# Optimization experiments

Hardware: AMD Instinct MI355X
Metric: run time of the kernel (lower is better)

Reference implementation:

```python
import jax, jax.numpy as jnp
import numpy as np

DIM = 256
NUM_RFS = 256
OUT_DIM = 1024
N = 65536
M = 0.001


def setup_inputs() -> dict:
    key = jax.random.key(0)
    k1, k2, k3, k4, k5, k6 = jax.random.split(key, 6)
    x = jax.random.normal(k1, (N, DIM), dtype=jnp.float32)
    input_weights = jax.random.normal(k2, (OUT_DIM, DIM), dtype=jnp.float32)
    b = jax.random.normal(k3, (OUT_DIM,), dtype=jnp.float32)
    # projection matrix: normal(mean=0, std=0.02, size=(num_rfs, dim))
    proj = 0.02 * jax.random.normal(k4, (NUM_RFS, DIM), dtype=jnp.float32)
    # xis are complex points of the random-feature construction; keep small for exp stability
    xis_real = 0.1 * jax.random.normal(k5, (NUM_RFS,), dtype=jnp.float32)
    xis_imag = 0.1 * jax.random.normal(k6, (NUM_RFS,), dtype=jnp.float32)
    return {"x": x, "input_weights": input_weights, "b": b, "proj": proj,
            "xis_real": xis_real, "xis_imag": xis_imag}


def _asym_feats(xw, xis, proj, bias, is_weight):
    """create_asym_feats with a_fun/b_fun = identity, A_fun/B_fun = exp(xi*b).
    xw: (rows, DIM) float; xis: (NUM_RFS,) complex64; proj: (NUM_RFS, DIM) float.
    Returns (rows, NUM_RFS) complex64."""
    ab = xis  # ab_fun is identity -> ab_coeffs = xis
    scale = np.sqrt(1.0 + 4.0 * M).astype(np.float32)
    # renorm_gs[i] = sqrt(1+4M) * ab[i] * gs[i]  -> (NUM_RFS, DIM) complex
    renorm_gs = scale * ab[:, None] * proj.astype(jnp.complex64)
    # dot_products = xw_c @ renorm_gs.T  -> (rows, NUM_RFS) complex
    dot = jnp.einsum('nd,rd->nr', xw.astype(jnp.complex64), renorm_gs)
    sq = jnp.sum(xw * xw, axis=-1)  # (rows,)
    # correction: outer(sq/2, ab*ab) + M*||g_i||^2 (broadcast over rows)
    corr = (sq[:, None] * 0.5) * (ab * ab)[None, :]
    corr = corr + M * jnp.sum(proj * proj, axis=-1)[None, :]
    feats = jnp.exp(dot - corr) * np.float32(1.0 / np.sqrt(NUM_RFS))
    if is_weight:
        # AB_coeffs[j, i] = exp(xis[i] * bias[j])
        AB = jnp.exp(xis[None, :] * bias[:, None].astype(jnp.complex64))
        feats = AB * feats
    return feats


def reference(x, input_weights, b, proj, xis_real, xis_imag):
    xis = (xis_real + 1j * xis_imag).astype(jnp.complex64)
    # normalize=False path: scale weights and bias by dim**-0.25 at init time
    inv4 = np.float32(1.0 / DIM ** 0.25)
    w = input_weights * inv4
    bb = b * inv4
    c = np.float32((1.0 / np.sqrt(2.0)) * (1.0 + 4.0 * M) ** (DIM / 4.0))
    # precomputed weight features (parameter of the module)
    w_plus = _asym_feats(w, xis, proj, bb, is_weight=True)
    w_minus = _asym_feats(w, -xis, proj, bb, is_weight=True)
    weights = c * jnp.concatenate([w_plus, w_minus], axis=-1)  # (OUT_DIM, 2R) complex
    # forward: x scaled by 1/dim (normalize=False)
    xs = x * np.float32(1.0 / DIM)
    f_plus = _asym_feats(xs, xis, proj, bb, is_weight=False)
    f_minus = _asym_feats(xs, -xis, proj, bb, is_weight=False)
    feat = c * jnp.concatenate([f_plus, f_minus], axis=-1)  # (N, 2R) complex
    # (feat @ weights.T).real
    out = jnp.einsum('nr,or->no', feat, weights).real
    return out
```

## Files before the change

kernel.cpp:

```cpp
#include <hip/hip_runtime.h>
#include <cmath>
#include <cstdint>

#define NROWS 65536
#define DIMN  256
#define NRF   256
#define OUTD  1024
#define KDIM  1024
#define MCOEF 0.001f

typedef __bf16 v8bf __attribute__((ext_vector_type(8)));
typedef float  v4f  __attribute__((ext_vector_type(4)));

__device__ __forceinline__ unsigned short f2bf(float f) {
  unsigned int u = __float_as_uint(f);
  u += 0x7fffu + ((u >> 16) & 1u);
  return (unsigned short)(u >> 16);
}

__device__ __forceinline__ void async_copy16(const void* g, void* l) {
  __builtin_amdgcn_global_load_lds(
      (const __attribute__((address_space(1))) void*)g,
      (__attribute__((address_space(3))) void*)l, 16, 0, 0);
}

__global__ __launch_bounds__(256) void prep_rows(
    const float* __restrict__ src, unsigned short* __restrict__ dst,
    float* __restrict__ sqout, float scl, int rows) {
  int row  = blockIdx.x * 4 + (threadIdx.x >> 6);
  int lane = threadIdx.x & 63;
  if (row >= rows) return;
  float4 v = ((const float4*)(src + (size_t)row * DIMN))[lane];
  v.x *= scl; v.y *= scl; v.z *= scl; v.w *= scl;
  float ss = v.x * v.x + v.y * v.y + v.z * v.z + v.w * v.w;
  ushort4 o;
  o.x = f2bf(v.x); o.y = f2bf(v.y); o.z = f2bf(v.z); o.w = f2bf(v.w);
  ((ushort4*)(dst + (size_t)row * DIMN))[lane] = o;
#pragma unroll
  for (int off = 32; off > 0; off >>= 1) ss += __shfl_down(ss, off, 64);
  if (lane == 0) sqout[row] = ss;
}

__global__ __launch_bounds__(64) void prep_rf(
    const float* __restrict__ proj, unsigned short* __restrict__ projbf,
    float* __restrict__ mg2) {
  int i = blockIdx.x;
  int lane = threadIdx.x;
  float4 v = ((const float4*)(proj + (size_t)i * DIMN))[lane];
  ushort4 o;
  o.x = f2bf(v.x); o.y = f2bf(v.y); o.z = f2bf(v.z); o.w = f2bf(v.w);
  ((ushort4*)(projbf + (size_t)i * DIMN))[lane] = o;
  float ss = v.x * v.x + v.y * v.y + v.z * v.z + v.w * v.w;
#pragma unroll
  for (int off = 32; off > 0; off >>= 1) ss += __shfl_down(ss, off, 64);
  if (lane == 0) mg2[i] = MCOEF * ss;
}

__global__ __launch_bounds__(256) void fused_features(
    const unsigned short* __restrict__ Am,
    const float* __restrict__ sq,
    const float* __restrict__ bias,
    float bscl,
    const float* __restrict__ xr_g, const float* __restrict__ xi_g,
    const float* __restrict__ mg2_g,
    const unsigned short* __restrict__ projbf,
    unsigned short* __restrict__ Fout,
    float sR, float sI, float scaleC) {
  __shared__ __align__(16) unsigned short As[64 * 32];
  __shared__ __align__(16) unsigned short Bs[256 * 32];
  __shared__ float xr_s[256], xi_s[256], c1_s[256], c2_s[256], mg2_s[256];
  __shared__ float sq_s[64], bias_s[64];

  int t = threadIdx.x;
  int lane = t & 63;
  int w = t >> 6;
  int blockRow = blockIdx.x * 64;

  {
    float a = xr_g[t], b = xi_g[t];
    xr_s[t] = a; xi_s[t] = b;
    c1_s[t] = a * a - b * b;
    c2_s[t] = 2.f * a * b;
    mg2_s[t] = mg2_g[t];
  }
  if (t < 64) {
    int r = blockRow + t;
    sq_s[t] = sq[r];
    bias_s[t] = bias ? bias[r] * bscl : 0.f;
  }

  v4f acc[4][4];
#pragma unroll
  for (int a = 0; a < 4; a++)
#pragma unroll
    for (int b = 0; b < 4; b++)
#pragma unroll
      for (int q = 0; q < 4; q++) acc[a][b][q] = 0.f;

  for (int kb = 0; kb < DIMN; kb += 32) {
    {
      int idx = t;
      int row = idx >> 2, kc = (idx & 3) * 8;
      async_copy16(Am + (size_t)(blockRow + row) * DIMN + kb + kc,
                   As + (idx & ~63) * 8);
    }
#pragma unroll
    for (int r = 0; r < 4; r++) {
      int idx = r * 256 + t;
      int row = idx >> 2, kc = (idx & 3) * 8;
      async_copy16(projbf + (size_t)row * DIMN + kb + kc,
                   Bs + (idx & ~63) * 8);
    }
    __syncthreads();
    v8bf af[4], bfv[4];
#pragma unroll
    for (int mi = 0; mi < 4; mi++)
      af[mi] = *(const v8bf*)&As[(mi * 16 + (lane & 15)) * 32 + (lane >> 4) * 8];
#pragma unroll
    for (int ni = 0; ni < 4; ni++)
      bfv[ni] = *(const v8bf*)&Bs[(w * 64 + ni * 16 + (lane & 15)) * 32 + (lane >> 4) * 8];
#pragma unroll
    for (int mi = 0; mi < 4; mi++)
#pragma unroll
      for (int ni = 0; ni < 4; ni++)
        acc[mi][ni] = __builtin_amdgcn_mfma_f32_16x16x32_bf16(
            af[mi], bfv[ni], acc[mi][ni], 0, 0, 0);
    __syncthreads();
  }

#pragma unroll
  for (int mi = 0; mi < 4; mi++) {
#pragma unroll
    for (int ni = 0; ni < 4; ni++) {
#pragma unroll
      for (int reg = 0; reg < 4; reg++) {
        int rloc = mi * 16 + (lane >> 4) * 4 + reg;
        int i    = w * 64 + ni * 16 + (lane & 15);
        float px = acc[mi][ni][reg];
        float tt = scaleC * px + bias_s[rloc];
        float u  = 0.5f * sq_s[rloc];
        float aa = u * c1_s[i] + mg2_s[i];
        float bb = u * c2_s[i];
        float txr = tt * xr_s[i];
        float txi = tt * xi_s[i];
        float erp = __expf(txr - aa);
        float erm = __expf(-txr - aa);
        float s1, cc1, s2, cc2;
        __sincosf(txi - bb, &s1, &cc1);
        __sincosf(txi + bb, &s2, &cc2);
        unsigned short* o = Fout + (size_t)(blockRow + rloc) * KDIM;
        o[i]             = f2bf(sR * erp * cc1);
        o[NRF + i]       = f2bf(sR * erm * cc2);
        o[2 * NRF + i]   = f2bf(sI * erp * s1);
        o[3 * NRF + i]   = f2bf(-sI * erm * s2);
      }
    }
  }
}

__global__ __launch_bounds__(256) void gemm_bt(
    const unsigned short* __restrict__ A,
    const unsigned short* __restrict__ B,
    float* __restrict__ C) {
  __shared__ __align__(16) unsigned short As[128 * 32];
  __shared__ __align__(16) unsigned short Bs[128 * 32];
  int t = threadIdx.x;
  int lane = t & 63;
  int w = t >> 6;
  int wm = w >> 1, wn = w & 1;
  size_t bm = (size_t)blockIdx.y * 128;
  size_t bn = (size_t)blockIdx.x * 128;

  v4f acc[4][4];
#pragma unroll
  for (int a = 0; a < 4; a++)
#pragma unroll
    for (int b = 0; b < 4; b++)
#pragma unroll
      for (int q = 0; q < 4; q++) acc[a][b][q] = 0.f;

  for (int kb = 0; kb < KDIM; kb += 32) {
#pragma unroll
    for (int r = 0; r < 2; r++) {
      int idx = r * 256 + t;
      int row = idx >> 2, kc = (idx & 3) * 8;
      async_copy16(A + (bm + row) * KDIM + kb + kc, As + (idx & ~63) * 8);
      async_copy16(B + (bn + row) * KDIM + kb + kc, Bs + (idx & ~63) * 8);
    }
    __syncthreads();
    v8bf af[4], bfv[4];
#pragma unroll
    for (int mi = 0; mi < 4; mi++)
      af[mi] = *(const v8bf*)&As[(wm * 64 + mi * 16 + (lane & 15)) * 32 + (lane >> 4) * 8];
#pragma unroll
    for (int ni = 0; ni < 4; ni++)
      bfv[ni] = *(const v8bf*)&Bs[(wn * 64 + ni * 16 + (lane & 15)) * 32 + (lane >> 4) * 8];
#pragma unroll
    for (int mi = 0; mi < 4; mi++)
#pragma unroll
      for (int ni = 0; ni < 4; ni++)
        acc[mi][ni] = __builtin_amdgcn_mfma_f32_16x16x32_bf16(
            af[mi], bfv[ni], acc[mi][ni], 0, 0, 0);
    __syncthreads();
  }

#pragma unroll
  for (int mi = 0; mi < 4; mi++)
#pragma unroll
    for (int ni = 0; ni < 4; ni++)
#pragma unroll
      for (int reg = 0; reg < 4; reg++) {
        size_t row = bm + wm * 64 + mi * 16 + (lane >> 4) * 4 + reg;
        size_t col = bn + wn * 64 + ni * 16 + (lane & 15);
        C[row * OUTD + col] = acc[mi][ni][reg];
      }
}

extern "C" void kernel_launch(void* const* d_in, const int* in_sizes, int n_in,
                              void* d_out, int out_size, void* d_ws, size_t ws_size,
                              hipStream_t stream) {
  (void)in_sizes; (void)n_in; (void)out_size;
  const float* x    = (const float*)d_in[0];
  const float* iw   = (const float*)d_in[1];
  const float* bvec = (const float*)d_in[2];
  const float* proj = (const float*)d_in[3];
  const float* xr   = (const float*)d_in[4];
  const float* xi   = (const float*)d_in[5];
  float* out = (float*)d_out;

  char* ws = (char*)d_ws;
  size_t off = 0;
  auto take = [&](size_t bytes) {
    char* p = ws + off;
    off = (off + bytes + 255) & ~(size_t)255;
    return p;
  };
  unsigned short* F      = (unsigned short*)take((size_t)NROWS * KDIM * 2);
  unsigned short* xs     = (unsigned short*)take((size_t)NROWS * DIMN * 2);
  unsigned short* Wp     = (unsigned short*)take((size_t)OUTD * KDIM * 2);
  unsigned short* wmb    = (unsigned short*)take((size_t)OUTD * DIMN * 2);
  unsigned short* projbf = (unsigned short*)take((size_t)NRF * DIMN * 2);
  float* sqx = (float*)take((size_t)NROWS * 4);
  float* sqw = (float*)take((size_t)OUTD * 4);
  float* mg2 = (float*)take((size_t)NRF * 4);
  if (ws_size < off) return;

  const float  scaleC = sqrtf(1.f + 4.f * MCOEF);
  const double c2d    = 0.5 * exp(128.0 * log(1.0 + 4.0 * 0.001));
  const float  invSR  = 0.0625f;
  const float  sRw    = (float)(c2d * 0.0625);

  prep_rows<<<NROWS / 4, 256, 0, stream>>>(x, xs, sqx, 1.f / DIMN, NROWS);
  prep_rows<<<OUTD / 4, 256, 0, stream>>>(iw, wmb, sqw, 0.25f, OUTD);
  prep_rf<<<NRF, 64, 0, stream>>>(proj, projbf, mg2);
  fused_features<<<NROWS / 64, 256, 0, stream>>>(
      xs, sqx, nullptr, 0.f, xr, xi, mg2, projbf, F, invSR, invSR, scaleC);
  fused_features<<<OUTD / 64, 256, 0, stream>>>(
      wmb, sqw, bvec, 0.25f, xr, xi, mg2, projbf, Wp, sRw, -sRw, scaleC);
  gemm_bt<<<dim3(8, 512), 256, 0, stream>>>(F, Wp, out);
}
```

Measured before the change: 586.1 us.

## Fuse row prep into feature kernel, stage output in LDS, remap GEMM blocks

Removes the prep_rows kernels: fused_features now reads fp32 rows directly, scales them, converts to bf16 into LDS and accumulates the squared norm in registers. Feature outputs are staged in a 32KB LDS buffer per 16-row slab and written out as coalesced 16-byte stores instead of scattered 2-byte stores. The GEMM launch becomes a 1D grid with a remapped block order so that concurrently running blocks share B tiles and nearby A rows. This trades some extra syncs and LDS usage, which may lower occupancy, for less global traffic and fewer launches.

```diff
diff --git a/kernel.cpp b/kernel.cpp
--- a/kernel.cpp
+++ b/kernel.cpp
@@ -11,6 +11,7 @@
 
 typedef __bf16 v8bf __attribute__((ext_vector_type(8)));
 typedef float  v4f  __attribute__((ext_vector_type(4)));
+typedef unsigned short us8 __attribute__((ext_vector_type(8)));
 
 __device__ __forceinline__ unsigned short f2bf(float f) {
   unsigned int u = __float_as_uint(f);
@@ -22,23 +23,6 @@
   __builtin_amdgcn_global_load_lds(
       (const __attribute__((address_space(1))) void*)g,
       (__attribute__((address_space(3))) void*)l, 16, 0, 0);
-}
-
-__global__ __launch_bounds__(256) void prep_rows(
-    const float* __restrict__ src, unsigned short* __restrict__ dst,
-    float* __restrict__ sqout, float scl, int rows) {
-  int row  = blockIdx.x * 4 + (threadIdx.x >> 6);
-  int lane = threadIdx.x & 63;
-  if (row >= rows) return;
-  float4 v = ((const float4*)(src + (size_t)row * DIMN))[lane];
-  v.x *= scl; v.y *= scl; v.z *= scl; v.w *= scl;
-  float ss = v.x * v.x + v.y * v.y + v.z * v.z + v.w * v.w;
-  ushort4 o;
-  o.x = f2bf(v.x); o.y = f2bf(v.y); o.z = f2bf(v.z); o.w = f2bf(v.w);
-  ((ushort4*)(dst + (size_t)row * DIMN))[lane] = o;
-#pragma unroll
-  for (int off = 32; off > 0; off >>= 1) ss += __shfl_down(ss, off, 64);
-  if (lane == 0) sqout[row] = ss;
 }
 
 __global__ __launch_bounds__(64) void prep_rf(
@@ -57,8 +41,8 @@
 }
 
 __global__ __launch_bounds__(256) void fused_features(
-    const unsigned short* __restrict__ Am,
-    const float* __restrict__ sq,
+    const float* __restrict__ src,
+    float scl,
     const float* __restrict__ bias,
     float bscl,
     const float* __restrict__ xr_g, const float* __restrict__ xi_g,
@@ -66,8 +50,10 @@
     const unsigned short* __restrict__ projbf,
     unsigned short* __restrict__ Fout,
     float sR, float sI, float scaleC) {
-  __shared__ __align__(16) unsigned short As[64 * 32];
-  __shared__ __align__(16) unsigned short Bs[256 * 32];
+  __shared__ __align__(16) unsigned short big[16 * 1024];
+  unsigned short* As = big;
+  unsigned short* Bs = big + 2048;
+  unsigned short* Os = big;
   __shared__ float xr_s[256], xi_s[256], c1_s[256], c2_s[256], mg2_s[256];
   __shared__ float sq_s[64], bias_s[64];
 
@@ -83,11 +69,7 @@
     c2_s[t] = 2.f * a * b;
     mg2_s[t] = mg2_g[t];
   }
-  if (t < 64) {
-    int r = blockRow + t;
-    sq_s[t] = sq[r];
-    bias_s[t] = bias ? bias[r] * bscl : 0.f;
-  }
+  if (t < 64) bias_s[t] = bias ? bias[blockRow + t] * bscl : 0.f;
 
   v4f acc[4][4];
 #pragma unroll
@@ -97,13 +79,21 @@
 #pragma unroll
       for (int q = 0; q < 4; q++) acc[a][b][q] = 0.f;
 
+  int arow = t >> 2, sub = t & 3;
+  const float* srow = src + (size_t)(blockRow + arow) * DIMN + sub * 8;
+  float ss = 0.f;
+
   for (int kb = 0; kb < DIMN; kb += 32) {
-    {
-      int idx = t;
-      int row = idx >> 2, kc = (idx & 3) * 8;
-      async_copy16(Am + (size_t)(blockRow + row) * DIMN + kb + kc,
-                   As + (idx & ~63) * 8);
-    }
+    float4 v0 = *(const float4*)(srow + kb);
+    float4 v1 = *(const float4*)(srow + kb + 4);
+    v0.x *= scl; v0.y *= scl; v0.z *= scl; v0.w *= scl;
+    v1.x *= scl; v1.y *= scl; v1.z *= scl; v1.w *= scl;
+    ss += v0.x * v0.x + v0.y * v0.y + v0.z * v0.z + v0.w * v0.w +
+          v1.x * v1.x + v1.y * v1.y + v1.z * v1.z + v1.w * v1.w;
+    us8 o;
+    o[0] = f2bf(v0.x); o[1] = f2bf(v0.y); o[2] = f2bf(v0.z); o[3] = f2bf(v0.w);
+    o[4] = f2bf(v1.x); o[5] = f2bf(v1.y); o[6] = f2bf(v1.z); o[7] = f2bf(v1.w);
+    *(us8*)&As[arow * 32 + sub * 8] = o;
 #pragma unroll
     for (int r = 0; r < 4; r++) {
       int idx = r * 256 + t;
@@ -128,17 +118,23 @@
     __syncthreads();
   }
 
+  ss += __shfl_xor(ss, 1, 64);
+  ss += __shfl_xor(ss, 2, 64);
+  if (sub == 0) sq_s[arow] = ss;
+
 #pragma unroll
   for (int mi = 0; mi < 4; mi++) {
+    __syncthreads();
 #pragma unroll
     for (int ni = 0; ni < 4; ni++) {
 #pragma unroll
       for (int reg = 0; reg < 4; reg++) {
-        int rloc = mi * 16 + (lane >> 4) * 4 + reg;
-        int i    = w * 64 + ni * 16 + (lane & 15);
+        int rl    = (lane >> 4) * 4 + reg;
+        int rglob = mi * 16 + rl;
+        int i     = w * 64 + ni * 16 + (lane & 15);
         float px = acc[mi][ni][reg];
-        float tt = scaleC * px + bias_s[rloc];
-        float u  = 0.5f * sq_s[rloc];
+        float tt = scaleC * px + bias_s[rglob];
+        float u  = 0.5f * sq_s[rglob];
         float aa = u * c1_s[i] + mg2_s[i];
         float bb = u * c2_s[i];
         float txr = tt * xr_s[i];
@@ -148,12 +144,20 @@
         float s1, cc1, s2, cc2;
         __sincosf(txi - bb, &s1, &cc1);
         __sincosf(txi + bb, &s2, &cc2);
-        unsigned short* o = Fout + (size_t)(blockRow + rloc) * KDIM;
-        o[i]             = f2bf(sR * erp * cc1);
-        o[NRF + i]       = f2bf(sR * erm * cc2);
-        o[2 * NRF + i]   = f2bf(sI * erp * s1);
-        o[3 * NRF + i]   = f2bf(-sI * erm * s2);
+        Os[rl * KDIM + i]            = f2bf(sR * erp * cc1);
+        Os[rl * KDIM + NRF + i]      = f2bf(sR * erm * cc2);
+        Os[rl * KDIM + 2 * NRF + i]  = f2bf(sI * erp * s1);
+        Os[rl * KDIM + 3 * NRF + i]  = f2bf(-sI * erm * s2);
       }
+    }
+    __syncthreads();
+#pragma unroll
+    for (int j = 0; j < 8; j++) {
+      int chunk = j * 256 + t;
+      int rowo  = chunk >> 7;
+      int off   = (chunk & 127) * 8;
+      *(us8*)(Fout + (size_t)(blockRow + mi * 16 + rowo) * KDIM + off) =
+          *(const us8*)&Os[rowo * KDIM + off];
     }
   }
 }
@@ -168,8 +172,10 @@
   int lane = t & 63;
   int w = t >> 6;
   int wm = w >> 1, wn = w & 1;
-  size_t bm = (size_t)blockIdx.y * 128;
-  size_t bn = (size_t)blockIdx.x * 128;
+  int lid = blockIdx.x;
+  int slot = lid >> 3;
+  size_t bm = (size_t)(((lid & 7) * 64) + (slot >> 3)) * 128;
+  size_t bn = (size_t)(slot & 7) * 128;
 
   v4f acc[4][4];
 #pragma unroll
@@ -236,12 +242,8 @@
     return p;
   };
   unsigned short* F      = (unsigned short*)take((size_t)NROWS * KDIM * 2);
-  unsigned short* xs     = (unsigned short*)take((size_t)NROWS * DIMN * 2);
   unsigned short* Wp     = (unsigned short*)take((size_t)OUTD * KDIM * 2);
-  unsigned short* wmb    = (unsigned short*)take((size_t)OUTD * DIMN * 2);
   unsigned short* projbf = (unsigned short*)take((size_t)NRF * DIMN * 2);
-  float* sqx = (float*)take((size_t)NROWS * 4);
-  float* sqw = (float*)take((size_t)OUTD * 4);
   float* mg2 = (float*)take((size_t)NRF * 4);
   if (ws_size < off) return;
 
@@ -250,12 +252,10 @@
   const float  invSR  = 0.0625f;
   const float  sRw    = (float)(c2d * 0.0625);
 
-  prep_rows<<<NROWS / 4, 256, 0, stream>>>(x, xs, sqx, 1.f / DIMN, NROWS);
-  prep_rows<<<OUTD / 4, 256, 0, stream>>>(iw, wmb, sqw, 0.25f, OUTD);
   prep_rf<<<NRF, 64, 0, stream>>>(proj, projbf, mg2);
   fused_features<<<NROWS / 64, 256, 0, stream>>>(
-      xs, sqx, nullptr, 0.f, xr, xi, mg2, projbf, F, invSR, invSR, scaleC);
+      x, 1.f / DIMN, nullptr, 0.f, xr, xi, mg2, projbf, F, invSR, invSR, scaleC);
   fused_features<<<OUTD / 64, 256, 0, stream>>>(
-      wmb, sqw, bvec, 0.25f, xr, xi, mg2, projbf, Wp, sRw, -sRw, scaleC);
-  gemm_bt<<<dim3(8, 512), 256, 0, stream>>>(F, Wp, out);
-}
+      iw, 0.25f, bvec, 0.25f, xr, xi, mg2, projbf, Wp, sRw, -sRw, scaleC);
+  gemm_bt<<<4096, 256, 0, stream>>>(F, Wp, out);
+}
```

Measured after the change: 570.2 us. 2.7% less time.
